# Kernel optimization log

Measured on AMD Instinct MI355X. Metric: run time of the kernel, lower is better.

The kernel has to match this reference:

```python
import jax, jax.numpy as jnp
import numpy as np

B, L, D_MODEL, N_HEADS = 2, 1024, 1024, 8
KH = D_MODEL // 2 // N_HEADS   # key head dim = 64
VH = D_MODEL // N_HEADS        # value head dim = 128
SCALING = KH ** -0.5


def setup_inputs() -> dict:
    key = jax.random.key(0)
    ks = jax.random.split(key, 9)
    def w(k, shp):
        return jax.random.normal(k, shp, dtype=jnp.float32) / np.float32(np.sqrt(shp[0]))
    return {
        "x": jax.random.normal(ks[0], (B, L, D_MODEL), dtype=jnp.float32),
        "Wq": w(ks[1], (D_MODEL, D_MODEL // 2)),
        "Wk": w(ks[2], (D_MODEL, D_MODEL // 2)),
        "Wg1": w(ks[3], (D_MODEL, 16)),
        "Wg2": w(ks[4], (16, D_MODEL // 2)),
        "Wv": w(ks[5], (D_MODEL, D_MODEL)),
        "Wgp": w(ks[6], (D_MODEL, D_MODEL)),
        "bgp": jnp.zeros((D_MODEL,), jnp.float32),
        "Wout": w(ks[7], (D_MODEL, D_MODEL)),
    }


def _split_heads(t):
    # (b, l, h*d) -> (b, h, l, d)
    b, l, _ = t.shape
    return t.reshape(b, l, N_HEADS, -1).transpose(0, 2, 1, 3)


def _forward(x, Wq, Wk, Wg1, Wg2, Wv, Wgp, bgp, Wout):
    q = _split_heads(x @ Wq)                    # b h l kd
    k = _split_heads(x @ Wk) * SCALING          # b h l kd
    kg = _split_heads((x @ Wg1) @ Wg2)          # b h l kd (low-rank gate)
    v = _split_heads(x @ Wv)                    # b h l vd
    g = jax.nn.silu(x @ Wgp + bgp)              # b l d
    # per-head scalar decay gate in (0,1)
    gate = jnp.exp(jnp.mean(jax.nn.log_sigmoid(kg), axis=-1, keepdims=True) / 16.0)  # b h l 1
    prefix = jnp.cumprod(gate + 1e-6, axis=2)[..., None]                              # b h l 1 1
    kv = jnp.einsum('bhld,bhle->bhlde', k, v)                                         # b h l kd vd
    state = jnp.cumsum(kv / prefix, axis=2) * prefix                                  # decayed running KV state
    out = jnp.einsum('bhld,bhlde->bhle', q, state)                                    # b h l vd
    # LayerNorm over value head dim, no affine, eps=1e-5
    mu = out.mean(-1, keepdims=True)
    var = out.var(-1, keepdims=True)
    out = (out - mu) * jax.lax.rsqrt(var + 1e-5)
    out = out.transpose(0, 2, 1, 3).reshape(x.shape[0], x.shape[1], D_MODEL)
    return (g * out) @ Wout


def reference(x, Wq, Wk, Wg1, Wg2, Wv, Wgp, bgp, Wout):
    return _forward(x, Wq, Wk, Wg1, Wg2, Wv, Wgp, bgp, Wout)
```

## Files before the change

kernel.cpp:

```cpp
#include <hip/hip_runtime.h>

typedef __bf16 bf16x8 __attribute__((ext_vector_type(8)));
typedef float floatx4 __attribute__((ext_vector_type(4)));

__device__ __forceinline__ ushort f2bf(float f) {
  union { float f; unsigned u; } a; a.f = f;
  unsigned u = a.u;
  unsigned r = (u + 0x7FFFu + ((u >> 16) & 1u)) >> 16;
  return (ushort)r;
}
__device__ __forceinline__ float bf2f(ushort u) {
  union { unsigned u; float f; } a; a.u = ((unsigned)u) << 16;
  return a.f;
}

__device__ __forceinline__ void gl_lds16(const ushort* g, ushort* l) {
  __builtin_amdgcn_global_load_lds((const __attribute__((address_space(1))) void*)g,
                                   (__attribute__((address_space(3))) void*)l, 16, 0, 0);
}

#define SWZH(row, col, stride) ((((row) * (stride)) + (col)) ^ (((row) & 7) << 3))
#define SWZC(row, col) ((((row) * 128) + (col)) ^ ((((row) >> 3) & 7) << 2))

__global__ __launch_bounds__(256) void conv_all_kernel(
    const float* __restrict__ Wq, const float* __restrict__ Wk,
    const float* __restrict__ Wv, const float* __restrict__ Wgp,
    const float* __restrict__ Wout,
    ushort* __restrict__ WcatT, ushort* __restrict__ WoutT) {
  int nv = blockIdx.x * 32, k0 = blockIdx.y * 32;
  const float* W; ushort* dst; int N, ncol, nrow; float scale = 1.f;
  if (nv < 512)       { W = Wq;   N = 512;  ncol = nv;         nrow = nv;        dst = WcatT; }
  else if (nv < 1024) { W = Wk;   N = 512;  ncol = nv - 512;   nrow = nv;        dst = WcatT; scale = 0.125f; }
  else if (nv < 2048) { W = Wv;   N = 1024; ncol = nv - 1024;  nrow = nv;        dst = WcatT; }
  else if (nv < 3072) { W = Wgp;  N = 1024; ncol = nv - 2048;  nrow = nv;        dst = WcatT; }
  else                { W = Wout; N = 1024; ncol = nv - 3072;  nrow = nv - 3072; dst = WoutT; }
  __shared__ float tile[32][33];
  int xi = threadIdx.x & 31, yi = threadIdx.x >> 5;
  #pragma unroll
  for (int i = 0; i < 32; i += 8)
    tile[yi + i][xi] = W[(size_t)(k0 + yi + i) * N + ncol + xi];
  __syncthreads();
  #pragma unroll
  for (int i = 0; i < 32; i += 8)
    dst[(size_t)(nrow + yi + i) * 1024 + k0 + xi] = f2bf(tile[xi][yi + i] * scale);
}

__global__ __launch_bounds__(256) void gate_kernel(const float* __restrict__ x,
                                                   const float* __restrict__ Wg1,
                                                   const float* __restrict__ Wg2,
                                                   float* __restrict__ gamma,
                                                   ushort* __restrict__ xb) {
  int rowi = blockIdx.x;
  int b = rowi >> 10, l = rowi & 1023;
  int tid = threadIdx.x;
  __shared__ float part[16][17];
  __shared__ float tsh[16];

  {
    float4 v = *(const float4*)(x + (size_t)rowi * 1024 + tid * 4);
    ushort4 o;
    o.x = f2bf(v.x); o.y = f2bf(v.y); o.z = f2bf(v.z); o.w = f2bf(v.w);
    *(ushort4*)(xb + (size_t)rowi * 1024 + tid * 4) = o;
  }

  {
    int j = tid & 15, slice = tid >> 4;
    const float* xr = x + (size_t)rowi * 1024 + slice * 64;
    float p = 0.f;
    #pragma unroll 4
    for (int kk = 0; kk < 64; kk++)
      p += xr[kk] * Wg1[(size_t)(slice * 64 + kk) * 16 + j];
    part[slice][j] = p;
  }
  __syncthreads();
  if (tid < 16) {
    float s = 0.f;
    #pragma unroll
    for (int i = 0; i < 16; i++) s += part[i][tid];
    tsh[tid] = s;
  }
  __syncthreads();

  float ls0, ls1;
  {
    int n = tid;
    float kg = 0.f;
    #pragma unroll
    for (int j = 0; j < 16; j++) kg += tsh[j] * Wg2[j * 512 + n];
    ls0 = (kg >= 0.f) ? -log1pf(expf(-kg)) : (kg - log1pf(expf(kg)));
  }
  {
    int n = tid + 256;
    float kg = 0.f;
    #pragma unroll
    for (int j = 0; j < 16; j++) kg += tsh[j] * Wg2[j * 512 + n];
    ls1 = (kg >= 0.f) ? -log1pf(expf(-kg)) : (kg - log1pf(expf(kg)));
  }
  #pragma unroll
  for (int m = 32; m >= 1; m >>= 1) {
    ls0 += __shfl_xor(ls0, m);
    ls1 += __shfl_xor(ls1, m);
  }
  if ((tid & 63) == 0) {
    int w = tid >> 6;
    gamma[(size_t)(b * 8 + w) * 1024 + l]       = expf(ls0 * (1.f / 1024.f)) + 1e-6f;
    gamma[(size_t)(b * 8 + w + 4) * 1024 + l]   = expf(ls1 * (1.f / 1024.f)) + 1e-6f;
  }
}

__global__ __launch_bounds__(64) void prefix_kernel(const float* __restrict__ gamma,
                                                    float* __restrict__ af,
                                                    float* __restrict__ Atot) {
  int blk = blockIdx.x;
  int bh = blk >> 4, c = blk & 15;
  int lane = threadIdx.x;
  float g = gamma[(size_t)bh * 1024 + c * 64 + lane];
  #pragma unroll
  for (int m = 1; m < 64; m <<= 1) {
    float o = __shfl_up(g, m);
    if (lane >= m) g *= o;
  }
  af[(size_t)bh * 1024 + c * 64 + lane] = g;
  if (lane == 63) Atot[blk] = g;
}

__global__ __launch_bounds__(256) void gemm_proj_kernel(
    const ushort* __restrict__ A, const ushort* __restrict__ BT,
    const float* __restrict__ af, const float* __restrict__ Atot,
    const float* __restrict__ bgp,
    ushort* __restrict__ Qb, ushort* __restrict__ Kb,
    ushort* __restrict__ Ktb, ushort* __restrict__ Vtb,
    ushort* __restrict__ gsilu) {
  const int K = 1024;
  __shared__ __align__(16) char ldsraw[32768];
  ushort* As = (ushort*)ldsraw;
  ushort* Bs = (ushort*)(ldsraw + 8192);
  float*  Cs = (float*)ldsraw;
  __shared__ float ssh[2][64];
  __shared__ float bsh[128];

  int tid = threadIdx.x;
  int lane = tid & 63, wid = tid >> 6;
  int wr = wid >> 1, wc = wid & 1;
  int m0 = blockIdx.x * 64, n0 = blockIdx.y * 128;
  int by = blockIdx.y;
  int rtype = (by < 4) ? 0 : (by < 8) ? 1 : (by < 16) ? 2 : 3;
  int b = m0 >> 10, lbase = m0 & 1023, cch = lbase >> 6;

  if (rtype <= 1) {
    if (tid < 128) {
      int j = tid >> 6, li = tid & 63;
      int h = ((n0 - (rtype << 9)) >> 6) + j;
      int bh = b * 8 + h;
      float a = af[(size_t)bh * 1024 + lbase + li];
      ssh[j][li] = (rtype == 0) ? a : (Atot[bh * 16 + cch] / a);
    }
  } else if (rtype == 3) {
    if (tid < 128) bsh[tid] = bgp[n0 - 2048 + tid];
  }

  floatx4 acc[2][4];
  #pragma unroll
  for (int r = 0; r < 2; r++)
    #pragma unroll
    for (int c = 0; c < 4; c++)
      acc[r][c] = (floatx4){0.f, 0.f, 0.f, 0.f};

  int srA = wid * 16 + (lane >> 3);
  int srB = wid * 32 + (lane >> 3);
  int sc = (lane & 7) * 8;
  const ushort* ag = A + (size_t)(m0 + srA) * K + sc;
  const ushort* bg = BT + (size_t)(n0 + srB) * K + sc;
  ushort* asb = As + (wid * 16) * 64;
  ushort* bsb = Bs + (wid * 32) * 64;
  int row = lane & 15, kseg = (lane >> 4) << 3;

  for (int k0 = 0; k0 < K; k0 += 64) {
    __syncthreads();
    #pragma unroll
    for (int i = 0; i < 2; i++)
      gl_lds16(ag + (size_t)(i * 8) * K + k0, asb + i * 8 * 64);
    #pragma unroll
    for (int i = 0; i < 4; i++)
      gl_lds16(bg + (size_t)(i * 8) * K + k0, bsb + i * 8 * 64);
    __syncthreads();
    #pragma unroll
    for (int kk = 0; kk < 64; kk += 32) {
      bf16x8 av[2], bv[4];
      #pragma unroll
      for (int r = 0; r < 2; r++)
        av[r] = *(const bf16x8*)&As[(wr * 32 + r * 16 + row) * 64 + kk + kseg];
      #pragma unroll
      for (int c = 0; c < 4; c++)
        bv[c] = *(const bf16x8*)&Bs[(wc * 64 + c * 16 + row) * 64 + kk + kseg];
      #pragma unroll
      for (int r = 0; r < 2; r++)
        #pragma unroll
        for (int c = 0; c < 4; c++)
          acc[r][c] = __builtin_amdgcn_mfma_f32_16x16x32_bf16(av[r], bv[c], acc[r][c], 0, 0, 0);
    }
  }

  __syncthreads();
  #pragma unroll
  for (int r = 0; r < 2; r++) {
    int crow = wr * 32 + r * 16 + ((lane >> 4) << 2);
    #pragma unroll
    for (int c = 0; c < 4; c++) {
      int ccol = wc * 64 + c * 16 + (lane & 15);
      #pragma unroll
      for (int i = 0; i < 4; i++)
        Cs[SWZC(crow + i, ccol)] = acc[r][c][i];
    }
  }
  __syncthreads();

  if (rtype == 0) {
    #pragma unroll
    for (int it = 0; it < 4; it++) {
      int u = tid + it * 256;
      int rw = u >> 4, col8 = (u & 15) * 8;
      int hh = col8 >> 6, d = col8 & 63;
      float a = ssh[hh][rw];
      float4 v0 = *(const float4*)&Cs[SWZC(rw, col8)];
      float4 v1 = *(const float4*)&Cs[SWZC(rw, col8 + 4)];
      ushort o[8];
      o[0]=f2bf(v0.x*a); o[1]=f2bf(v0.y*a); o[2]=f2bf(v0.z*a); o[3]=f2bf(v0.w*a);
      o[4]=f2bf(v1.x*a); o[5]=f2bf(v1.y*a); o[6]=f2bf(v1.z*a); o[7]=f2bf(v1.w*a);
      int bh = b * 8 + (n0 >> 6) + hh;
      *(uint4*)(Qb + ((size_t)bh * 1024 + lbase + rw) * 64 + d) = *(uint4*)&o[0];
    }
  } else if (rtype == 1) {
    #pragma unroll
    for (int it = 0; it < 4; it++) {
      int u = tid + it * 256;
      int rw = u >> 4, col8 = (u & 15) * 8;
      int hh = col8 >> 6, d = col8 & 63;
      float4 v0 = *(const float4*)&Cs[SWZC(rw, col8)];
      float4 v1 = *(const float4*)&Cs[SWZC(rw, col8 + 4)];
      ushort o[8];
      o[0]=f2bf(v0.x); o[1]=f2bf(v0.y); o[2]=f2bf(v0.z); o[3]=f2bf(v0.w);
      o[4]=f2bf(v1.x); o[5]=f2bf(v1.y); o[6]=f2bf(v1.z); o[7]=f2bf(v1.w);
      int bh = b * 8 + ((n0 - 512) >> 6) + hh;
      *(uint4*)(Kb + ((size_t)bh * 1024 + lbase + rw) * 64 + d) = *(uint4*)&o[0];
    }
    #pragma unroll
    for (int it = 0; it < 4; it++) {
      int u = tid + it * 256;
      int l0 = (u & 7) * 8, dd = (u >> 3) & 63, hh = u >> 9;
      ushort o[8];
      #pragma unroll
      for (int j = 0; j < 8; j++)
        o[j] = f2bf(Cs[SWZC(l0 + j, hh * 64 + dd)] * ssh[hh][l0 + j]);
      int bh = b * 8 + ((n0 - 512) >> 6) + hh;
      *(uint4*)(Ktb + ((size_t)(bh * 64 + dd)) * 1024 + lbase + l0) = *(uint4*)&o[0];
    }
  } else if (rtype == 2) {
    #pragma unroll
    for (int it = 0; it < 4; it++) {
      int u = tid + it * 256;
      int l0 = (u & 7) * 8, e = u >> 3;
      ushort o[8];
      #pragma unroll
      for (int j = 0; j < 8; j++)
        o[j] = f2bf(Cs[SWZC(l0 + j, e)]);
      int bh = b * 8 + ((n0 - 1024) >> 7);
      *(uint4*)(Vtb + ((size_t)(bh * 128 + e)) * 1024 + lbase + l0) = *(uint4*)&o[0];
    }
  } else {
    #pragma unroll
    for (int it = 0; it < 4; it++) {
      int u = tid + it * 256;
      int rw = u >> 4, col8 = (u & 15) * 8;
      float4 v0 = *(const float4*)&Cs[SWZC(rw, col8)];
      float4 v1 = *(const float4*)&Cs[SWZC(rw, col8 + 4)];
      float vv[8] = {v0.x, v0.y, v0.z, v0.w, v1.x, v1.y, v1.z, v1.w};
      ushort o[8];
      #pragma unroll
      for (int j = 0; j < 8; j++) {
        float z = vv[j] + bsh[col8 + j];
        o[j] = f2bf(z / (1.f + expf(-z)));
      }
      *(uint4*)(gsilu + (size_t)(m0 + rw) * 1024 + (n0 - 2048) + col8) = *(uint4*)&o[0];
    }
  }
}

__global__ __launch_bounds__(256) void gemm_out_kernel(const ushort* __restrict__ A,
                                                       const ushort* __restrict__ BT,
                                                       float* __restrict__ C) {
  const int K = 1024, N = 1024;
  __shared__ __align__(16) ushort As[64 * 64];
  __shared__ __align__(16) ushort Bs[128 * 64];
  int tid = threadIdx.x;
  int lane = tid & 63, wid = tid >> 6;
  int wr = wid >> 1, wc = wid & 1;
  int m0 = blockIdx.x * 64, n0 = blockIdx.y * 128;
  int row = lane & 15, kseg = (lane >> 4) << 3;

  floatx4 acc[2][4];
  #pragma unroll
  for (int r = 0; r < 2; r++)
    #pragma unroll
    for (int c = 0; c < 4; c++)
      acc[r][c] = (floatx4){0.f, 0.f, 0.f, 0.f};

  int srowA = wid * 16 + (lane >> 3);
  int srowB = wid * 32 + (lane >> 3);
  int scol = (lane & 7) * 8;
  const ushort* ag = A + (size_t)(m0 + srowA) * K + scol;
  const ushort* bg = BT + (size_t)(n0 + srowB) * K + scol;
  ushort* asb = As + (wid * 16) * 64;
  ushort* bsb = Bs + (wid * 32) * 64;

  for (int k0 = 0; k0 < K; k0 += 64) {
    __syncthreads();
    #pragma unroll
    for (int i = 0; i < 2; i++)
      gl_lds16(ag + (size_t)(i * 8) * K + k0, asb + i * 8 * 64);
    #pragma unroll
    for (int i = 0; i < 4; i++)
      gl_lds16(bg + (size_t)(i * 8) * K + k0, bsb + i * 8 * 64);
    __syncthreads();
    #pragma unroll
    for (int kk = 0; kk < 64; kk += 32) {
      bf16x8 av[2], bv[4];
      #pragma unroll
      for (int r = 0; r < 2; r++)
        av[r] = *(const bf16x8*)&As[(wr * 32 + r * 16 + row) * 64 + kk + kseg];
      #pragma unroll
      for (int c = 0; c < 4; c++)
        bv[c] = *(const bf16x8*)&Bs[(wc * 64 + c * 16 + row) * 64 + kk + kseg];
      #pragma unroll
      for (int r = 0; r < 2; r++)
        #pragma unroll
        for (int c = 0; c < 4; c++)
          acc[r][c] = __builtin_amdgcn_mfma_f32_16x16x32_bf16(av[r], bv[c], acc[r][c], 0, 0, 0);
    }
  }

  int r4 = (lane >> 4) << 2;
  #pragma unroll
  for (int r = 0; r < 2; r++)
    #pragma unroll
    for (int c = 0; c < 4; c++) {
      int crow = m0 + wr * 32 + r * 16 + r4;
      int ccol = n0 + wc * 64 + c * 16 + (lane & 15);
      #pragma unroll
      for (int i = 0; i < 4; i++)
        C[(size_t)(crow + i) * N + ccol] = acc[r][c][i];
    }
}

__global__ __launch_bounds__(256) void chunk_T_kernel(const ushort* __restrict__ Ktb,
                                                      const ushort* __restrict__ Vtb,
                                                      float* __restrict__ Tt) {
  int c = blockIdx.x, bh = blockIdx.y;
  int tid = threadIdx.x;
  int lane = tid & 63, wid = tid >> 6;
  int col_l = lane & 15, kseg8 = (lane >> 4) * 8;
  int d0w = wid * 16;

  __shared__ __align__(16) ushort Kt[64 * 64];
  __shared__ __align__(16) ushort Vs[128 * 64];

  #pragma unroll
  for (int i = 0; i < 2; i++) {
    int u = tid + i * 256;
    int row = u >> 3, col8 = u & 7;
    *(uint4*)&Kt[SWZH(row, col8 * 8, 64)] =
        *(const uint4*)(Ktb + ((size_t)(bh * 64 + row)) * 1024 + c * 64 + col8 * 8);
  }
  #pragma unroll
  for (int i = 0; i < 4; i++) {
    int u = tid + i * 256;
    int row = u >> 3, col8 = u & 7;
    *(uint4*)&Vs[SWZH(row, col8 * 8, 64)] =
        *(const uint4*)(Vtb + ((size_t)(bh * 128 + row)) * 1024 + c * 64 + col8 * 8);
  }
  __syncthreads();

  floatx4 acc[8];
  #pragma unroll
  for (int i = 0; i < 8; i++) acc[i] = (floatx4){0.f, 0.f, 0.f, 0.f};

  #pragma unroll
  for (int kk = 0; kk < 64; kk += 32) {
    bf16x8 kb = *(const bf16x8*)&Kt[SWZH(d0w + col_l, kk + kseg8, 64)];
    #pragma unroll
    for (int fe = 0; fe < 8; fe++) {
      bf16x8 vb = *(const bf16x8*)&Vs[SWZH(fe * 16 + col_l, kk + kseg8, 64)];
      acc[fe] = __builtin_amdgcn_mfma_f32_16x16x32_bf16(vb, kb, acc[fe], 0, 0, 0);
    }
  }

  float* To = Tt + (size_t)(bh * 16 + c) * 8192;
  #pragma unroll
  for (int fe = 0; fe < 8; fe++) {
    #pragma unroll
    for (int r = 0; r < 4; r++) {
      int e = fe * 16 + (lane >> 4) * 4 + r;
      To[(size_t)e * 64 + d0w + col_l] = acc[fe][r];
    }
  }
}

__global__ __launch_bounds__(256) void state_kernel(const float* __restrict__ Tt,
                                                    const float* __restrict__ Atot,
                                                    ushort* __restrict__ Stb) {
  int es = blockIdx.x, bh = blockIdx.y;
  int tid = threadIdx.x;
  size_t off = (size_t)es * 512 + tid * 2;
  float2 S = {0.f, 0.f};
  for (int c = 0; c < 16; c++) {
    float A = Atot[bh * 16 + c];
    size_t base = (size_t)(bh * 16 + c) * 8192 + off;
    ushort2 o; o.x = f2bf(S.x); o.y = f2bf(S.y);
    *(ushort2*)(Stb + base) = o;
    float2 t = *(const float2*)(Tt + base);
    S.x = A * S.x + t.x;
    S.y = A * S.y + t.y;
  }
}

__global__ __launch_bounds__(256) void out_chunk_kernel(const float* __restrict__ af,
                                                        const ushort* __restrict__ Qb,
                                                        const ushort* __restrict__ Kb,
                                                        const ushort* __restrict__ Stb,
                                                        const ushort* __restrict__ Vtb,
                                                        const ushort* __restrict__ gsilu,
                                                        ushort* __restrict__ gout) {
  int c = blockIdx.x, bh = blockIdx.y;
  int b = bh >> 3, h = bh & 7;
  int tid = threadIdx.x;
  int lane = tid & 63, wid = tid >> 6;
  int col_l = lane & 15, kseg8 = (lane >> 4) * 8;
  int t0w = wid * 16;

  __shared__ __align__(16) ushort Qs[64 * 64];
  __shared__ __align__(16) ushort Ks[64 * 64];
  __shared__ __align__(16) ushort Ss[128 * 64];
  __shared__ __align__(16) ushort Vs[128 * 64];
  __shared__ __align__(16) ushort Ps[64 * 64];
  __shared__ __align__(16) ushort Gz[64 * 128];
  __shared__ float inva_sh[64];

  #pragma unroll
  for (int i = 0; i < 2; i++) {
    int u = tid + i * 256;
    int row = u >> 3, col8 = u & 7;
    *(uint4*)&Qs[SWZH(row, col8 * 8, 64)] =
        *(const uint4*)(Qb + ((size_t)(bh * 1024 + c * 64 + row)) * 64 + col8 * 8);
    *(uint4*)&Ks[SWZH(row, col8 * 8, 64)] =
        *(const uint4*)(Kb + ((size_t)(bh * 1024 + c * 64 + row)) * 64 + col8 * 8);
  }
  #pragma unroll
  for (int i = 0; i < 4; i++) {
    int u = tid + i * 256;
    int row = u >> 3, col8 = u & 7;
    *(uint4*)&Ss[SWZH(row, col8 * 8, 64)] =
        *(const uint4*)(Stb + (size_t)(bh * 16 + c) * 8192 + (size_t)row * 64 + col8 * 8);
    *(uint4*)&Vs[SWZH(row, col8 * 8, 64)] =
        *(const uint4*)(Vtb + ((size_t)(bh * 128 + row)) * 1024 + c * 64 + col8 * 8);
  }
  #pragma unroll
  for (int i = 0; i < 4; i++) {
    int u = tid + i * 256;
    int row = u >> 4, ch = u & 15;
    *(uint4*)&Gz[SWZH(row, ch * 8, 128)] =
        *(const uint4*)(gsilu + ((size_t)(b * 1024 + c * 64 + row)) * 1024 + h * 128 + ch * 8);
  }
  if (tid < 64) inva_sh[tid] = 1.f / af[(size_t)bh * 1024 + c * 64 + tid];
  __syncthreads();

  floatx4 pacc[4];
  floatx4 acc[8];
  #pragma unroll
  for (int i = 0; i < 4; i++) pacc[i] = (floatx4){0.f, 0.f, 0.f, 0.f};
  #pragma unroll
  for (int i = 0; i < 8; i++) acc[i] = (floatx4){0.f, 0.f, 0.f, 0.f};

  #pragma unroll
  for (int kk = 0; kk < 64; kk += 32) {
    bf16x8 qb = *(const bf16x8*)&Qs[SWZH(t0w + col_l, kk + kseg8, 64)];
    #pragma unroll
    for (int fs = 0; fs < 4; fs++) {
      bf16x8 kb = *(const bf16x8*)&Ks[SWZH(fs * 16 + col_l, kk + kseg8, 64)];
      pacc[fs] = __builtin_amdgcn_mfma_f32_16x16x32_bf16(kb, qb, pacc[fs], 0, 0, 0);
    }
    #pragma unroll
    for (int fe = 0; fe < 8; fe++) {
      bf16x8 sb = *(const bf16x8*)&Ss[SWZH(fe * 16 + col_l, kk + kseg8, 64)];
      acc[fe] = __builtin_amdgcn_mfma_f32_16x16x32_bf16(sb, qb, acc[fe], 0, 0, 0);
    }
  }

  int tl = t0w + col_l;
  #pragma unroll
  for (int fs = 0; fs < 4; fs++) {
    ushort o[4];
    #pragma unroll
    for (int r = 0; r < 4; r++) {
      int s = fs * 16 + (lane >> 4) * 4 + r;
      float pv = (s <= tl) ? pacc[fs][r] * inva_sh[s] : 0.f;
      o[r] = f2bf(pv);
    }
    int s0 = fs * 16 + (lane >> 4) * 4;
    *(ushort4*)&Ps[SWZH(tl, s0, 64)] = *(ushort4*)&o[0];
  }
  __syncthreads();

  #pragma unroll
  for (int kk = 0; kk < 64; kk += 32) {
    bf16x8 pb = *(const bf16x8*)&Ps[SWZH(t0w + col_l, kk + kseg8, 64)];
    #pragma unroll
    for (int fe = 0; fe < 8; fe++) {
      bf16x8 vb = *(const bf16x8*)&Vs[SWZH(fe * 16 + col_l, kk + kseg8, 64)];
      acc[fe] = __builtin_amdgcn_mfma_f32_16x16x32_bf16(vb, pb, acc[fe], 0, 0, 0);
    }
  }
  __syncthreads();

  float s1 = 0.f, s2 = 0.f;
  #pragma unroll
  for (int fe = 0; fe < 8; fe++)
    #pragma unroll
    for (int r = 0; r < 4; r++) {
      float v = acc[fe][r];
      s1 += v; s2 += v * v;
    }
  s1 += __shfl_xor(s1, 16); s2 += __shfl_xor(s2, 16);
  s1 += __shfl_xor(s1, 32); s2 += __shfl_xor(s2, 32);
  float mu = s1 * (1.f / 128.f);
  float var = s2 * (1.f / 128.f) - mu * mu;
  float rs = rsqrtf(var + 1e-5f);

  ushort* Gs = Vs;
  #pragma unroll
  for (int fe = 0; fe < 8; fe++)
    #pragma unroll
    for (int r = 0; r < 4; r++) {
      int e = fe * 16 + (lane >> 4) * 4 + r;
      float y = (acc[fe][r] - mu) * rs;
      float g = bf2f(Gz[SWZH(tl, e, 128)]);
      Gs[SWZH(tl, e, 128)] = f2bf(y * g);
    }
  __syncthreads();

  #pragma unroll
  for (int i = 0; i < 4; i++) {
    int u = tid + i * 256;
    int row = u >> 4, ch = u & 15;
    *(uint4*)(gout + ((size_t)(b * 1024 + c * 64 + row)) * 1024 + h * 128 + ch * 8) =
        *(uint4*)&Gs[SWZH(row, ch * 8, 128)];
  }
}

extern "C" void kernel_launch(void* const* d_in, const int* in_sizes, int n_in,
                              void* d_out, int out_size, void* d_ws, size_t ws_size,
                              hipStream_t stream) {
  const float* x    = (const float*)d_in[0];
  const float* Wq   = (const float*)d_in[1];
  const float* Wk   = (const float*)d_in[2];
  const float* Wg1  = (const float*)d_in[3];
  const float* Wg2  = (const float*)d_in[4];
  const float* Wv   = (const float*)d_in[5];
  const float* Wgp  = (const float*)d_in[6];
  const float* bgp  = (const float*)d_in[7];
  const float* Wout = (const float*)d_in[8];
  float* out = (float*)d_out;

  char* ws = (char*)d_ws;
  float*  Tt     = (float*)(ws + 0);
  ushort* Stb    = (ushort*)(ws + 8388608);
  float*  gamma  = (float*)(ws + 12582912);
  float*  af     = (float*)(ws + 12648448);
  float*  Atot   = (float*)(ws + 12713984);
  ushort* Qb     = (ushort*)(ws + 12718080);
  ushort* Kb     = (ushort*)(ws + 14815232);
  ushort* Ktb    = (ushort*)(ws + 16912384);
  ushort* Vtb    = (ushort*)(ws + 19009536);
  ushort* xb     = (ushort*)(ws + 23203840);
  ushort* WcatT  = (ushort*)(ws + 27398144);
  ushort* WoutT  = (ushort*)(ws + 33689600);
  ushort* gout   = (ushort*)(ws + 35786752);
  ushort* gsilu  = (ushort*)(ws + 39981056);

  conv_all_kernel<<<dim3(128, 32), 256, 0, stream>>>(Wq, Wk, Wv, Wgp, Wout, WcatT, WoutT);
  gate_kernel<<<2048, 256, 0, stream>>>(x, Wg1, Wg2, gamma, xb);
  prefix_kernel<<<256, 64, 0, stream>>>(gamma, af, Atot);

  gemm_proj_kernel<<<dim3(32, 24), 256, 0, stream>>>(xb, WcatT, af, Atot, bgp,
                                                     Qb, Kb, Ktb, Vtb, gsilu);

  chunk_T_kernel<<<dim3(16, 16), 256, 0, stream>>>(Ktb, Vtb, Tt);
  state_kernel<<<dim3(16, 16), 256, 0, stream>>>(Tt, Atot, Stb);
  out_chunk_kernel<<<dim3(16, 16), 256, 0, stream>>>(af, Qb, Kb, Stb, Vtb, gsilu, gout);

  gemm_out_kernel<<<dim3(32, 8), 256, 0, stream>>>(gout, WoutT, out);
}
```

Measured before the change: 91.62 us.

## Fuse chunk scan kernels with grid barriers and merge weight-conversion with gate prep

Replaces the three chunked-scan kernels (chunk KV, state scan, output) with one persistent kernel of 256 blocks that uses atomic-counter grid barriers between phases, keeping the V tile resident in shared memory across phases. It also merges the weight transpose/convert kernel and the gate kernel into one launch, and stages the x row in shared memory for the Wg1 projection. The intent is to cut launch overhead and redundant reloads; the cost is a hipMemsetAsync per call and a reliance on all 256 blocks being co-resident, otherwise the spin barrier deadlocks.

```diff
diff --git a/kernel.cpp b/kernel.cpp
--- a/kernel.cpp
+++ b/kernel.cpp
@@ -22,61 +22,79 @@
 #define SWZH(row, col, stride) ((((row) * (stride)) + (col)) ^ (((row) & 7) << 3))
 #define SWZC(row, col) ((((row) * 128) + (col)) ^ ((((row) >> 3) & 7) << 2))
 
-__global__ __launch_bounds__(256) void conv_all_kernel(
+__device__ __forceinline__ void gbar(unsigned* ctr, unsigned target) {
+  __syncthreads();
+  __threadfence();
+  if (threadIdx.x == 0) {
+    atomicAdd(ctr, 1u);
+    while (__hip_atomic_load(ctr, __ATOMIC_ACQUIRE, __HIP_MEMORY_SCOPE_AGENT) < target)
+      __builtin_amdgcn_s_sleep(2);
+  }
+  __syncthreads();
+  __threadfence();
+}
+
+__global__ __launch_bounds__(256) void prep_all_kernel(
+    const float* __restrict__ x,
     const float* __restrict__ Wq, const float* __restrict__ Wk,
     const float* __restrict__ Wv, const float* __restrict__ Wgp,
     const float* __restrict__ Wout,
-    ushort* __restrict__ WcatT, ushort* __restrict__ WoutT) {
-  int nv = blockIdx.x * 32, k0 = blockIdx.y * 32;
-  const float* W; ushort* dst; int N, ncol, nrow; float scale = 1.f;
-  if (nv < 512)       { W = Wq;   N = 512;  ncol = nv;         nrow = nv;        dst = WcatT; }
-  else if (nv < 1024) { W = Wk;   N = 512;  ncol = nv - 512;   nrow = nv;        dst = WcatT; scale = 0.125f; }
-  else if (nv < 2048) { W = Wv;   N = 1024; ncol = nv - 1024;  nrow = nv;        dst = WcatT; }
-  else if (nv < 3072) { W = Wgp;  N = 1024; ncol = nv - 2048;  nrow = nv;        dst = WcatT; }
-  else                { W = Wout; N = 1024; ncol = nv - 3072;  nrow = nv - 3072; dst = WoutT; }
-  __shared__ float tile[32][33];
-  int xi = threadIdx.x & 31, yi = threadIdx.x >> 5;
-  #pragma unroll
-  for (int i = 0; i < 32; i += 8)
-    tile[yi + i][xi] = W[(size_t)(k0 + yi + i) * N + ncol + xi];
-  __syncthreads();
-  #pragma unroll
-  for (int i = 0; i < 32; i += 8)
-    dst[(size_t)(nrow + yi + i) * 1024 + k0 + xi] = f2bf(tile[xi][yi + i] * scale);
-}
-
-__global__ __launch_bounds__(256) void gate_kernel(const float* __restrict__ x,
-                                                   const float* __restrict__ Wg1,
-                                                   const float* __restrict__ Wg2,
-                                                   float* __restrict__ gamma,
-                                                   ushort* __restrict__ xb) {
-  int rowi = blockIdx.x;
+    const float* __restrict__ Wg1, const float* __restrict__ Wg2,
+    ushort* __restrict__ WcatT, ushort* __restrict__ WoutT,
+    float* __restrict__ gamma, ushort* __restrict__ xb) {
+  __shared__ __align__(16) float smem[1344];
+  int bid = blockIdx.x;
+  int tid = threadIdx.x;
+
+  if (bid < 4096) {
+    int nv = (bid & 127) * 32, k0 = (bid >> 7) * 32;
+    const float* W; ushort* dst; int N, ncol, nrow; float scale = 1.f;
+    if (nv < 512)       { W = Wq;   N = 512;  ncol = nv;         nrow = nv;        dst = WcatT; }
+    else if (nv < 1024) { W = Wk;   N = 512;  ncol = nv - 512;   nrow = nv;        dst = WcatT; scale = 0.125f; }
+    else if (nv < 2048) { W = Wv;   N = 1024; ncol = nv - 1024;  nrow = nv;        dst = WcatT; }
+    else if (nv < 3072) { W = Wgp;  N = 1024; ncol = nv - 2048;  nrow = nv;        dst = WcatT; }
+    else                { W = Wout; N = 1024; ncol = nv - 3072;  nrow = nv - 3072; dst = WoutT; }
+    float* tile = smem;
+    int xi = tid & 31, yi = tid >> 5;
+    #pragma unroll
+    for (int i = 0; i < 32; i += 8)
+      tile[(yi + i) * 33 + xi] = W[(size_t)(k0 + yi + i) * N + ncol + xi];
+    __syncthreads();
+    #pragma unroll
+    for (int i = 0; i < 32; i += 8)
+      dst[(size_t)(nrow + yi + i) * 1024 + k0 + xi] = f2bf(tile[xi * 33 + yi + i] * scale);
+    return;
+  }
+
+  int rowi = bid - 4096;
   int b = rowi >> 10, l = rowi & 1023;
-  int tid = threadIdx.x;
-  __shared__ float part[16][17];
-  __shared__ float tsh[16];
+  float* xrow = smem;
+  float* part = smem + 1024;
+  float* tsh  = smem + 1296;
 
   {
     float4 v = *(const float4*)(x + (size_t)rowi * 1024 + tid * 4);
     ushort4 o;
     o.x = f2bf(v.x); o.y = f2bf(v.y); o.z = f2bf(v.z); o.w = f2bf(v.w);
     *(ushort4*)(xb + (size_t)rowi * 1024 + tid * 4) = o;
-  }
+    *(float4*)&xrow[tid * 4] = v;
+  }
+  __syncthreads();
 
   {
     int j = tid & 15, slice = tid >> 4;
-    const float* xr = x + (size_t)rowi * 1024 + slice * 64;
+    const float* xr = xrow + slice * 64;
     float p = 0.f;
     #pragma unroll 4
     for (int kk = 0; kk < 64; kk++)
       p += xr[kk] * Wg1[(size_t)(slice * 64 + kk) * 16 + j];
-    part[slice][j] = p;
+    part[slice * 17 + j] = p;
   }
   __syncthreads();
   if (tid < 16) {
     float s = 0.f;
     #pragma unroll
-    for (int i = 0; i < 16; i++) s += part[i][tid];
+    for (int i = 0; i < 16; i++) s += part[i * 17 + tid];
     tsh[tid] = s;
   }
   __syncthreads();
@@ -286,6 +304,205 @@
   }
 }
 
+__global__ __launch_bounds__(256) void scan_fused_kernel(
+    const ushort* __restrict__ Ktb, const ushort* __restrict__ Vtb,
+    const float* __restrict__ Atot, const float* __restrict__ af,
+    const ushort* __restrict__ Qb, const ushort* __restrict__ Kb,
+    const ushort* __restrict__ gsilu,
+    float* __restrict__ Tt, ushort* __restrict__ Stb,
+    ushort* __restrict__ gout, unsigned* __restrict__ ctr) {
+  __shared__ __align__(16) ushort Vs[128 * 64];
+  __shared__ __align__(16) char uni[57344];
+  __shared__ float inva_sh[64];
+
+  int bx = blockIdx.x;
+  int c = bx & 15, bh = bx >> 4;
+  int b = bh >> 3, h = bh & 7;
+  int tid = threadIdx.x;
+  int lane = tid & 63, wid = tid >> 6;
+  int col_l = lane & 15, kseg8 = (lane >> 4) * 8;
+
+  {
+    ushort* Kt = (ushort*)uni;
+    #pragma unroll
+    for (int i = 0; i < 2; i++) {
+      int u = tid + i * 256;
+      int row = u >> 3, col8 = u & 7;
+      *(uint4*)&Kt[SWZH(row, col8 * 8, 64)] =
+          *(const uint4*)(Ktb + ((size_t)(bh * 64 + row)) * 1024 + c * 64 + col8 * 8);
+    }
+    #pragma unroll
+    for (int i = 0; i < 4; i++) {
+      int u = tid + i * 256;
+      int row = u >> 3, col8 = u & 7;
+      *(uint4*)&Vs[SWZH(row, col8 * 8, 64)] =
+          *(const uint4*)(Vtb + ((size_t)(bh * 128 + row)) * 1024 + c * 64 + col8 * 8);
+    }
+    __syncthreads();
+
+    int d0w = wid * 16;
+    floatx4 acc[8];
+    #pragma unroll
+    for (int i = 0; i < 8; i++) acc[i] = (floatx4){0.f, 0.f, 0.f, 0.f};
+
+    #pragma unroll
+    for (int kk = 0; kk < 64; kk += 32) {
+      bf16x8 kb = *(const bf16x8*)&Kt[SWZH(d0w + col_l, kk + kseg8, 64)];
+      #pragma unroll
+      for (int fe = 0; fe < 8; fe++) {
+        bf16x8 vb = *(const bf16x8*)&Vs[SWZH(fe * 16 + col_l, kk + kseg8, 64)];
+        acc[fe] = __builtin_amdgcn_mfma_f32_16x16x32_bf16(vb, kb, acc[fe], 0, 0, 0);
+      }
+    }
+
+    float* To = Tt + (size_t)(bh * 16 + c) * 8192;
+    #pragma unroll
+    for (int fe = 0; fe < 8; fe++) {
+      #pragma unroll
+      for (int r = 0; r < 4; r++) {
+        int e = fe * 16 + (lane >> 4) * 4 + r;
+        To[(size_t)e * 64 + d0w + col_l] = acc[fe][r];
+      }
+    }
+  }
+
+  gbar(ctr, 256);
+
+  {
+    int es = c;
+    size_t off = (size_t)es * 512 + tid * 2;
+    float2 S = {0.f, 0.f};
+    for (int cc = 0; cc < 16; cc++) {
+      float A = Atot[bh * 16 + cc];
+      size_t base = (size_t)(bh * 16 + cc) * 8192 + off;
+      ushort2 o; o.x = f2bf(S.x); o.y = f2bf(S.y);
+      *(ushort2*)(Stb + base) = o;
+      float2 t = *(const float2*)(Tt + base);
+      S.x = A * S.x + t.x;
+      S.y = A * S.y + t.y;
+    }
+  }
+
+  gbar(ctr + 1, 256);
+
+  {
+    ushort* Qs = (ushort*)uni;
+    ushort* Ks = (ushort*)(uni + 8192);
+    ushort* Ss = (ushort*)(uni + 16384);
+    ushort* Ps = (ushort*)(uni + 32768);
+    ushort* Gz = (ushort*)(uni + 40960);
+    int t0w = wid * 16;
+
+    #pragma unroll
+    for (int i = 0; i < 2; i++) {
+      int u = tid + i * 256;
+      int row = u >> 3, col8 = u & 7;
+      *(uint4*)&Qs[SWZH(row, col8 * 8, 64)] =
+          *(const uint4*)(Qb + ((size_t)(bh * 1024 + c * 64 + row)) * 64 + col8 * 8);
+      *(uint4*)&Ks[SWZH(row, col8 * 8, 64)] =
+          *(const uint4*)(Kb + ((size_t)(bh * 1024 + c * 64 + row)) * 64 + col8 * 8);
+    }
+    #pragma unroll
+    for (int i = 0; i < 4; i++) {
+      int u = tid + i * 256;
+      int row = u >> 3, col8 = u & 7;
+      *(uint4*)&Ss[SWZH(row, col8 * 8, 64)] =
+          *(const uint4*)(Stb + (size_t)(bh * 16 + c) * 8192 + (size_t)row * 64 + col8 * 8);
+    }
+    #pragma unroll
+    for (int i = 0; i < 4; i++) {
+      int u = tid + i * 256;
+      int row = u >> 4, ch = u & 15;
+      *(uint4*)&Gz[SWZH(row, ch * 8, 128)] =
+          *(const uint4*)(gsilu + ((size_t)(b * 1024 + c * 64 + row)) * 1024 + h * 128 + ch * 8);
+    }
+    if (tid < 64) inva_sh[tid] = 1.f / af[(size_t)bh * 1024 + c * 64 + tid];
+    __syncthreads();
+
+    floatx4 pacc[4];
+    floatx4 acc[8];
+    #pragma unroll
+    for (int i = 0; i < 4; i++) pacc[i] = (floatx4){0.f, 0.f, 0.f, 0.f};
+    #pragma unroll
+    for (int i = 0; i < 8; i++) acc[i] = (floatx4){0.f, 0.f, 0.f, 0.f};
+
+    #pragma unroll
+    for (int kk = 0; kk < 64; kk += 32) {
+      bf16x8 qb = *(const bf16x8*)&Qs[SWZH(t0w + col_l, kk + kseg8, 64)];
+      #pragma unroll
+      for (int fs = 0; fs < 4; fs++) {
+        bf16x8 kb = *(const bf16x8*)&Ks[SWZH(fs * 16 + col_l, kk + kseg8, 64)];
+        pacc[fs] = __builtin_amdgcn_mfma_f32_16x16x32_bf16(kb, qb, pacc[fs], 0, 0, 0);
+      }
+      #pragma unroll
+      for (int fe = 0; fe < 8; fe++) {
+        bf16x8 sb = *(const bf16x8*)&Ss[SWZH(fe * 16 + col_l, kk + kseg8, 64)];
+        acc[fe] = __builtin_amdgcn_mfma_f32_16x16x32_bf16(sb, qb, acc[fe], 0, 0, 0);
+      }
+    }
+
+    int tl = t0w + col_l;
+    #pragma unroll
+    for (int fs = 0; fs < 4; fs++) {
+      ushort o[4];
+      #pragma unroll
+      for (int r = 0; r < 4; r++) {
+        int s = fs * 16 + (lane >> 4) * 4 + r;
+        float pv = (s <= tl) ? pacc[fs][r] * inva_sh[s] : 0.f;
+        o[r] = f2bf(pv);
+      }
+      int s0 = fs * 16 + (lane >> 4) * 4;
+      *(ushort4*)&Ps[SWZH(tl, s0, 64)] = *(ushort4*)&o[0];
+    }
+    __syncthreads();
+
+    #pragma unroll
+    for (int kk = 0; kk < 64; kk += 32) {
+      bf16x8 pb = *(const bf16x8*)&Ps[SWZH(t0w + col_l, kk + kseg8, 64)];
+      #pragma unroll
+      for (int fe = 0; fe < 8; fe++) {
+        bf16x8 vb = *(const bf16x8*)&Vs[SWZH(fe * 16 + col_l, kk + kseg8, 64)];
+        acc[fe] = __builtin_amdgcn_mfma_f32_16x16x32_bf16(vb, pb, acc[fe], 0, 0, 0);
+      }
+    }
+    __syncthreads();
+
+    float s1 = 0.f, s2 = 0.f;
+    #pragma unroll
+    for (int fe = 0; fe < 8; fe++)
+      #pragma unroll
+      for (int r = 0; r < 4; r++) {
+        float v = acc[fe][r];
+        s1 += v; s2 += v * v;
+      }
+    s1 += __shfl_xor(s1, 16); s2 += __shfl_xor(s2, 16);
+    s1 += __shfl_xor(s1, 32); s2 += __shfl_xor(s2, 32);
+    float mu = s1 * (1.f / 128.f);
+    float var = s2 * (1.f / 128.f) - mu * mu;
+    float rs = rsqrtf(var + 1e-5f);
+
+    ushort* Gs = Vs;
+    #pragma unroll
+    for (int fe = 0; fe < 8; fe++)
+      #pragma unroll
+      for (int r = 0; r < 4; r++) {
+        int e = fe * 16 + (lane >> 4) * 4 + r;
+        float y = (acc[fe][r] - mu) * rs;
+        float g = bf2f(Gz[SWZH(tl, e, 128)]);
+        Gs[SWZH(tl, e, 128)] = f2bf(y * g);
+      }
+    __syncthreads();
+
+    #pragma unroll
+    for (int i = 0; i < 4; i++) {
+      int u = tid + i * 256;
+      int row = u >> 4, ch = u & 15;
+      *(uint4*)(gout + ((size_t)(b * 1024 + c * 64 + row)) * 1024 + h * 128 + ch * 8) =
+          *(uint4*)&Gs[SWZH(row, ch * 8, 128)];
+    }
+  }
+}
+
 __global__ __launch_bounds__(256) void gemm_out_kernel(const ushort* __restrict__ A,
                                                        const ushort* __restrict__ BT,
                                                        float* __restrict__ C) {
@@ -350,210 +567,6 @@
       for (int i = 0; i < 4; i++)
         C[(size_t)(crow + i) * N + ccol] = acc[r][c][i];
     }
-}
-
-__global__ __launch_bounds__(256) void chunk_T_kernel(const ushort* __restrict__ Ktb,
-                                                      const ushort* __restrict__ Vtb,
-                                                      float* __restrict__ Tt) {
-  int c = blockIdx.x, bh = blockIdx.y;
-  int tid = threadIdx.x;
-  int lane = tid & 63, wid = tid >> 6;
-  int col_l = lane & 15, kseg8 = (lane >> 4) * 8;
-  int d0w = wid * 16;
-
-  __shared__ __align__(16) ushort Kt[64 * 64];
-  __shared__ __align__(16) ushort Vs[128 * 64];
-
-  #pragma unroll
-  for (int i = 0; i < 2; i++) {
-    int u = tid + i * 256;
-    int row = u >> 3, col8 = u & 7;
-    *(uint4*)&Kt[SWZH(row, col8 * 8, 64)] =
-        *(const uint4*)(Ktb + ((size_t)(bh * 64 + row)) * 1024 + c * 64 + col8 * 8);
-  }
-  #pragma unroll
-  for (int i = 0; i < 4; i++) {
-    int u = tid + i * 256;
-    int row = u >> 3, col8 = u & 7;
-    *(uint4*)&Vs[SWZH(row, col8 * 8, 64)] =
-        *(const uint4*)(Vtb + ((size_t)(bh * 128 + row)) * 1024 + c * 64 + col8 * 8);
-  }
-  __syncthreads();
-
-  floatx4 acc[8];
-  #pragma unroll
-  for (int i = 0; i < 8; i++) acc[i] = (floatx4){0.f, 0.f, 0.f, 0.f};
-
-  #pragma unroll
-  for (int kk = 0; kk < 64; kk += 32) {
-    bf16x8 kb = *(const bf16x8*)&Kt[SWZH(d0w + col_l, kk + kseg8, 64)];
-    #pragma unroll
-    for (int fe = 0; fe < 8; fe++) {
-      bf16x8 vb = *(const bf16x8*)&Vs[SWZH(fe * 16 + col_l, kk + kseg8, 64)];
-      acc[fe] = __builtin_amdgcn_mfma_f32_16x16x32_bf16(vb, kb, acc[fe], 0, 0, 0);
-    }
-  }
-
-  float* To = Tt + (size_t)(bh * 16 + c) * 8192;
-  #pragma unroll
-  for (int fe = 0; fe < 8; fe++) {
-    #pragma unroll
-    for (int r = 0; r < 4; r++) {
-      int e = fe * 16 + (lane >> 4) * 4 + r;
-      To[(size_t)e * 64 + d0w + col_l] = acc[fe][r];
-    }
-  }
-}
-
-__global__ __launch_bounds__(256) void state_kernel(const float* __restrict__ Tt,
-                                                    const float* __restrict__ Atot,
-                                                    ushort* __restrict__ Stb) {
-  int es = blockIdx.x, bh = blockIdx.y;
-  int tid = threadIdx.x;
-  size_t off = (size_t)es * 512 + tid * 2;
-  float2 S = {0.f, 0.f};
-  for (int c = 0; c < 16; c++) {
-    float A = Atot[bh * 16 + c];
-    size_t base = (size_t)(bh * 16 + c) * 8192 + off;
-    ushort2 o; o.x = f2bf(S.x); o.y = f2bf(S.y);
-    *(ushort2*)(Stb + base) = o;
-    float2 t = *(const float2*)(Tt + base);
-    S.x = A * S.x + t.x;
-    S.y = A * S.y + t.y;
-  }
-}
-
-__global__ __launch_bounds__(256) void out_chunk_kernel(const float* __restrict__ af,
-                                                        const ushort* __restrict__ Qb,
-                                                        const ushort* __restrict__ Kb,
-                                                        const ushort* __restrict__ Stb,
-                                                        const ushort* __restrict__ Vtb,
-                                                        const ushort* __restrict__ gsilu,
-                                                        ushort* __restrict__ gout) {
-  int c = blockIdx.x, bh = blockIdx.y;
-  int b = bh >> 3, h = bh & 7;
-  int tid = threadIdx.x;
-  int lane = tid & 63, wid = tid >> 6;
-  int col_l = lane & 15, kseg8 = (lane >> 4) * 8;
-  int t0w = wid * 16;
-
-  __shared__ __align__(16) ushort Qs[64 * 64];
-  __shared__ __align__(16) ushort Ks[64 * 64];
-  __shared__ __align__(16) ushort Ss[128 * 64];
-  __shared__ __align__(16) ushort Vs[128 * 64];
-  __shared__ __align__(16) ushort Ps[64 * 64];
-  __shared__ __align__(16) ushort Gz[64 * 128];
-  __shared__ float inva_sh[64];
-
-  #pragma unroll
-  for (int i = 0; i < 2; i++) {
-    int u = tid + i * 256;
-    int row = u >> 3, col8 = u & 7;
-    *(uint4*)&Qs[SWZH(row, col8 * 8, 64)] =
-        *(const uint4*)(Qb + ((size_t)(bh * 1024 + c * 64 + row)) * 64 + col8 * 8);
-    *(uint4*)&Ks[SWZH(row, col8 * 8, 64)] =
-        *(const uint4*)(Kb + ((size_t)(bh * 1024 + c * 64 + row)) * 64 + col8 * 8);
-  }
-  #pragma unroll
-  for (int i = 0; i < 4; i++) {
-    int u = tid + i * 256;
-    int row = u >> 3, col8 = u & 7;
-    *(uint4*)&Ss[SWZH(row, col8 * 8, 64)] =
-        *(const uint4*)(Stb + (size_t)(bh * 16 + c) * 8192 + (size_t)row * 64 + col8 * 8);
-    *(uint4*)&Vs[SWZH(row, col8 * 8, 64)] =
-        *(const uint4*)(Vtb + ((size_t)(bh * 128 + row)) * 1024 + c * 64 + col8 * 8);
-  }
-  #pragma unroll
-  for (int i = 0; i < 4; i++) {
-    int u = tid + i * 256;
-    int row = u >> 4, ch = u & 15;
-    *(uint4*)&Gz[SWZH(row, ch * 8, 128)] =
-        *(const uint4*)(gsilu + ((size_t)(b * 1024 + c * 64 + row)) * 1024 + h * 128 + ch * 8);
-  }
-  if (tid < 64) inva_sh[tid] = 1.f / af[(size_t)bh * 1024 + c * 64 + tid];
-  __syncthreads();
-
-  floatx4 pacc[4];
-  floatx4 acc[8];
-  #pragma unroll
-  for (int i = 0; i < 4; i++) pacc[i] = (floatx4){0.f, 0.f, 0.f, 0.f};
-  #pragma unroll
-  for (int i = 0; i < 8; i++) acc[i] = (floatx4){0.f, 0.f, 0.f, 0.f};
-
-  #pragma unroll
-  for (int kk = 0; kk < 64; kk += 32) {
-    bf16x8 qb = *(const bf16x8*)&Qs[SWZH(t0w + col_l, kk + kseg8, 64)];
-    #pragma unroll
-    for (int fs = 0; fs < 4; fs++) {
-      bf16x8 kb = *(const bf16x8*)&Ks[SWZH(fs * 16 + col_l, kk + kseg8, 64)];
-      pacc[fs] = __builtin_amdgcn_mfma_f32_16x16x32_bf16(kb, qb, pacc[fs], 0, 0, 0);
-    }
-    #pragma unroll
-    for (int fe = 0; fe < 8; fe++) {
-      bf16x8 sb = *(const bf16x8*)&Ss[SWZH(fe * 16 + col_l, kk + kseg8, 64)];
-      acc[fe] = __builtin_amdgcn_mfma_f32_16x16x32_bf16(sb, qb, acc[fe], 0, 0, 0);
-    }
-  }
-
-  int tl = t0w + col_l;
-  #pragma unroll
-  for (int fs = 0; fs < 4; fs++) {
-    ushort o[4];
-    #pragma unroll
-    for (int r = 0; r < 4; r++) {
-      int s = fs * 16 + (lane >> 4) * 4 + r;
-      float pv = (s <= tl) ? pacc[fs][r] * inva_sh[s] : 0.f;
-      o[r] = f2bf(pv);
-    }
-    int s0 = fs * 16 + (lane >> 4) * 4;
-    *(ushort4*)&Ps[SWZH(tl, s0, 64)] = *(ushort4*)&o[0];
-  }
-  __syncthreads();
-
-  #pragma unroll
-  for (int kk = 0; kk < 64; kk += 32) {
-    bf16x8 pb = *(const bf16x8*)&Ps[SWZH(t0w + col_l, kk + kseg8, 64)];
-    #pragma unroll
-    for (int fe = 0; fe < 8; fe++) {
-      bf16x8 vb = *(const bf16x8*)&Vs[SWZH(fe * 16 + col_l, kk + kseg8, 64)];
-      acc[fe] = __builtin_amdgcn_mfma_f32_16x16x32_bf16(vb, pb, acc[fe], 0, 0, 0);
-    }
-  }
-  __syncthreads();
-
-  float s1 = 0.f, s2 = 0.f;
-  #pragma unroll
-  for (int fe = 0; fe < 8; fe++)
-    #pragma unroll
-    for (int r = 0; r < 4; r++) {
-      float v = acc[fe][r];
-      s1 += v; s2 += v * v;
-    }
-  s1 += __shfl_xor(s1, 16); s2 += __shfl_xor(s2, 16);
-  s1 += __shfl_xor(s1, 32); s2 += __shfl_xor(s2, 32);
-  float mu = s1 * (1.f / 128.f);
-  float var = s2 * (1.f / 128.f) - mu * mu;
-  float rs = rsqrtf(var + 1e-5f);
-
-  ushort* Gs = Vs;
-  #pragma unroll
-  for (int fe = 0; fe < 8; fe++)
-    #pragma unroll
-    for (int r = 0; r < 4; r++) {
-      int e = fe * 16 + (lane >> 4) * 4 + r;
-      float y = (acc[fe][r] - mu) * rs;
-      float g = bf2f(Gz[SWZH(tl, e, 128)]);
-      Gs[SWZH(tl, e, 128)] = f2bf(y * g);
-    }
-  __syncthreads();
-
-  #pragma unroll
-  for (int i = 0; i < 4; i++) {
-    int u = tid + i * 256;
-    int row = u >> 4, ch = u & 15;
-    *(uint4*)(gout + ((size_t)(b * 1024 + c * 64 + row)) * 1024 + h * 128 + ch * 8) =
-        *(uint4*)&Gs[SWZH(row, ch * 8, 128)];
-  }
 }
 
 extern "C" void kernel_launch(void* const* d_in, const int* in_sizes, int n_in,
@@ -585,17 +598,19 @@
   ushort* WoutT  = (ushort*)(ws + 33689600);
   ushort* gout   = (ushort*)(ws + 35786752);
   ushort* gsilu  = (ushort*)(ws + 39981056);
-
-  conv_all_kernel<<<dim3(128, 32), 256, 0, stream>>>(Wq, Wk, Wv, Wgp, Wout, WcatT, WoutT);
-  gate_kernel<<<2048, 256, 0, stream>>>(x, Wg1, Wg2, gamma, xb);
+  unsigned* ctr  = (unsigned*)(ws + 44175360);
+
+  hipMemsetAsync(ctr, 0, 8, stream);
+
+  prep_all_kernel<<<6144, 256, 0, stream>>>(x, Wq, Wk, Wv, Wgp, Wout, Wg1, Wg2,
+                                            WcatT, WoutT, gamma, xb);
   prefix_kernel<<<256, 64, 0, stream>>>(gamma, af, Atot);
 
   gemm_proj_kernel<<<dim3(32, 24), 256, 0, stream>>>(xb, WcatT, af, Atot, bgp,
                                                      Qb, Kb, Ktb, Vtb, gsilu);
 
-  chunk_T_kernel<<<dim3(16, 16), 256, 0, stream>>>(Ktb, Vtb, Tt);
-  state_kernel<<<dim3(16, 16), 256, 0, stream>>>(Tt, Atot, Stb);
-  out_chunk_kernel<<<dim3(16, 16), 256, 0, stream>>>(af, Qb, Kb, Stb, Vtb, gsilu, gout);
+  scan_fused_kernel<<<256, 256, 0, stream>>>(Ktb, Vtb, Atot, af, Qb, Kb, gsilu,
+                                             Tt, Stb, gout, ctr);
 
   gemm_out_kernel<<<dim3(32, 8), 256, 0, stream>>>(gout, WoutT, out);
 }
```

After: 202.4 us. +120.9%, slower.
